# Kernel optimization log

Measured on AMD Instinct MI355X. Metric: run time of the kernel, lower is better.

## Reference

```python
import jax, jax.numpy as jnp
import numpy as np
import math

EMBED_DIM = 512
D_K = 64
D_V = 64
B, S = 4, 4096


def setup_inputs() -> dict:
    key = jax.random.key(0)
    ks = jax.random.split(key, 9)
    s = 1.0 / math.sqrt(EMBED_DIM)
    return {
        "query_in": jax.random.normal(ks[0], (B, S, EMBED_DIM), jnp.float32),
        "key_in": jax.random.normal(ks[1], (B, S, EMBED_DIM), jnp.float32),
        "value_in": jax.random.normal(ks[2], (B, S, EMBED_DIM), jnp.float32),
        "Wq": jax.random.normal(ks[3], (EMBED_DIM, D_K), jnp.float32) * s,
        "bq": jnp.zeros((D_K,), jnp.float32),
        "Wk": jax.random.normal(ks[4], (EMBED_DIM, D_K), jnp.float32) * s,
        "bk": jnp.zeros((D_K,), jnp.float32),
        "Wv": jax.random.normal(ks[5], (EMBED_DIM, D_V), jnp.float32) * s,
        "bv": jnp.zeros((D_V,), jnp.float32),
    }


def reference(query_in, key_in, value_in, Wq, bq, Wk, bk, Wv, bv):
    # Linear projections (value computed for faithfulness; unused by the
    # truncated forward, which returns pre-softmax scaled scores)
    q = query_in @ Wq + bq            # [B,S,d_k]
    k = key_in @ Wk + bk              # [B,S,d_k]
    v = value_in @ Wv + bv            # [B,S,d_v] (unused downstream)
    # scaled dot-product scores: Q K^T / sqrt(d_k)  -> [B,S,S]
    scores = jnp.einsum("bqd,bkd->bqk", q, k) / math.sqrt(D_K)
    return scores
```

## Files before the change

### kernel.cpp

```cpp
#include <hip/hip_runtime.h>

constexpr int Bn = 4;
constexpr int S  = 4096;
constexpr int E  = 512;
constexpr int DK = 64;
constexpr int XS_STRIDE = DK + 8;

typedef __attribute__((ext_vector_type(8))) short   bf16x8;
typedef __attribute__((ext_vector_type(4))) float   f32x4;

__device__ __forceinline__ unsigned short f2bf(float f) {
    unsigned x = __builtin_bit_cast(unsigned, f);
    unsigned r = x + 0x7FFFu + ((x >> 16) & 1u);
    return (unsigned short)(r >> 16);
}

__device__ __forceinline__ bf16x8 load8_f2bf(const float* __restrict__ p) {
    f32x4 a = *(const f32x4*)p;
    f32x4 b = *(const f32x4*)(p + 4);
    bf16x8 o;
    o[0] = (short)f2bf(a[0]); o[1] = (short)f2bf(a[1]);
    o[2] = (short)f2bf(a[2]); o[3] = (short)f2bf(a[3]);
    o[4] = (short)f2bf(b[0]); o[5] = (short)f2bf(b[1]);
    o[6] = (short)f2bf(b[2]); o[7] = (short)f2bf(b[3]);
    return o;
}

__global__ __launch_bounds__(256) void wt_kernel(const float* __restrict__ Wq,
                                                 const float* __restrict__ Wk,
                                                 unsigned short* __restrict__ Wt) {
    int idx = blockIdx.x * 256 + threadIdx.x;
    const float* W = blockIdx.y ? Wk : Wq;
    int n = idx >> 9;
    int k = idx & 511;
    Wt[blockIdx.y * (DK * E) + idx] = f2bf(W[k * DK + n]);
}

__global__ __launch_bounds__(256) void proj_kernel(const float* __restrict__ Xq,
                                                   const float* __restrict__ Xk,
                                                   const unsigned short* __restrict__ Wt,
                                                   const float* __restrict__ bq,
                                                   const float* __restrict__ bk,
                                                   unsigned short* __restrict__ Qp,
                                                   unsigned short* __restrict__ Kp) {
    const float*          X    = blockIdx.y ? Xk : Xq;
    const unsigned short* Wtm  = Wt + (size_t)blockIdx.y * DK * E;
    const float*          bias = blockIdx.y ? bk : bq;
    unsigned short*       P    = blockIdx.y ? Kp : Qp;

    __shared__ unsigned short xs[32][XS_STRIDE];

    const int tid  = threadIdx.x;
    const int wave = tid >> 6;
    const int lane = tid & 63;
    const int quad = lane >> 4;
    const int l16  = lane & 15;
    const long row0 = (long)blockIdx.x * 32;

    const int wrt = (wave & 1) * 16;
    const int wct = (wave >> 1) * 32;

    const int sr = tid >> 3;
    const int sk = (tid & 7) * 8;
    const float* xsrc = &X[(row0 + sr) * E + sk];

    f32x4 acc[2];
    acc[0] = (f32x4){0.f, 0.f, 0.f, 0.f};
    acc[1] = (f32x4){0.f, 0.f, 0.f, 0.f};

    for (int k0 = 0; k0 < E; k0 += 64) {
        __syncthreads();
        *(bf16x8*)&xs[sr][sk] = load8_f2bf(xsrc + k0);
        __syncthreads();

        bf16x8 bfrag[2][2];
#pragma unroll
        for (int kc = 0; kc < 2; ++kc)
#pragma unroll
            for (int ct = 0; ct < 2; ++ct)
                bfrag[kc][ct] = *(const bf16x8*)&Wtm[(size_t)(wct + ct * 16 + l16) * E + k0 + kc * 32 + quad * 8];

#pragma unroll
        for (int kc = 0; kc < 2; ++kc) {
            bf16x8 af = *(const bf16x8*)&xs[wrt + l16][kc * 32 + quad * 8];
            acc[0] = __builtin_amdgcn_mfma_f32_16x16x32_bf16(af, bfrag[kc][0], acc[0], 0, 0, 0);
            acc[1] = __builtin_amdgcn_mfma_f32_16x16x32_bf16(af, bfrag[kc][1], acc[1], 0, 0, 0);
        }
    }

#pragma unroll
    for (int ct = 0; ct < 2; ++ct) {
        float bv = bias[wct + ct * 16 + l16];
#pragma unroll
        for (int r = 0; r < 4; ++r) {
            long row = row0 + wrt + quad * 4 + r;
            P[row * DK + wct + ct * 16 + l16] = f2bf(acc[ct][r] + bv);
        }
    }
}

__global__ __launch_bounds__(256) void score_kernel(const unsigned short* __restrict__ Q,
                                                    const unsigned short* __restrict__ K,
                                                    float* __restrict__ out) {
    __shared__ __align__(16) char smraw[2 * 128 * XS_STRIDE * 2];
    unsigned short (*qs)[XS_STRIDE] = (unsigned short(*)[XS_STRIDE])smraw;
    unsigned short (*ks)[XS_STRIDE] = (unsigned short(*)[XS_STRIDE])(smraw + 128 * XS_STRIDE * 2);

    const int tid  = threadIdx.x;
    const int wave = tid >> 6;
    const int lane = tid & 63;
    const int quad = lane >> 4;
    const int l16  = lane & 15;

    const int  b     = blockIdx.z;
    const long qrow0 = (long)blockIdx.y * 128;
    const long krow0 = (long)blockIdx.x * 128;
    const unsigned short* Qb = Q + (size_t)b * S * DK;
    const unsigned short* Kb = K + (size_t)b * S * DK;

#pragma unroll
    for (int c = tid; c < 1024; c += 256) {
        int r  = c >> 3;
        int kc = (c & 7) * 8;
        *(bf16x8*)&qs[r][kc] = *(const bf16x8*)&Qb[(qrow0 + r) * DK + kc];
        *(bf16x8*)&ks[r][kc] = *(const bf16x8*)&Kb[(krow0 + r) * DK + kc];
    }
    __syncthreads();

    const int wr = wave * 32;

    bf16x8 afrag[2][2];
#pragma unroll
    for (int rt = 0; rt < 2; ++rt)
#pragma unroll
        for (int kc = 0; kc < 2; ++kc)
            afrag[rt][kc] = *(const bf16x8*)&qs[wr + rt * 16 + l16][kc * 32 + quad * 8];

    f32x4 acc[2][8];
#pragma unroll
    for (int rt = 0; rt < 2; ++rt)
#pragma unroll
        for (int ct = 0; ct < 8; ++ct) acc[rt][ct] = (f32x4){0.f, 0.f, 0.f, 0.f};

#pragma unroll
    for (int ct = 0; ct < 8; ++ct) {
        bf16x8 b0 = *(const bf16x8*)&ks[ct * 16 + l16][quad * 8];
        bf16x8 b1 = *(const bf16x8*)&ks[ct * 16 + l16][32 + quad * 8];
#pragma unroll
        for (int rt = 0; rt < 2; ++rt) {
            acc[rt][ct] = __builtin_amdgcn_mfma_f32_16x16x32_bf16(afrag[rt][0], b0, acc[rt][ct], 0, 0, 0);
            acc[rt][ct] = __builtin_amdgcn_mfma_f32_16x16x32_bf16(afrag[rt][1], b1, acc[rt][ct], 0, 0, 0);
        }
    }

    __syncthreads();

    float (*wbuf)[132] = (float(*)[132])(smraw + (size_t)wave * (16 * 132 * 4));

    float* ob = out + (size_t)b * S * S;
    const int rrow = lane >> 3;
    const int rcol = (lane & 7) * 4;

#pragma unroll
    for (int rt = 0; rt < 2; ++rt) {
#pragma unroll
        for (int ct = 0; ct < 8; ++ct)
#pragma unroll
            for (int r = 0; r < 4; ++r)
                wbuf[quad * 4 + r][ct * 16 + l16] = acc[rt][ct][r] * 0.125f;

#pragma unroll
        for (int jr = 0; jr < 2; ++jr)
#pragma unroll
            for (int jc = 0; jc < 4; ++jc) {
                int rr = jr * 8 + rrow;
                int cc = jc * 32 + rcol;
                f32x4 v = *(const f32x4*)&wbuf[rr][cc];
                *(f32x4*)&ob[(qrow0 + wr + rt * 16 + rr) * S + krow0 + cc] = v;
            }
    }
}

extern "C" void kernel_launch(void* const* d_in, const int* in_sizes, int n_in,
                              void* d_out, int out_size, void* d_ws, size_t ws_size,
                              hipStream_t stream) {
    (void)in_sizes; (void)n_in; (void)out_size; (void)ws_size;

    const float* query = (const float*)d_in[0];
    const float* key   = (const float*)d_in[1];
    const float* Wq    = (const float*)d_in[3];
    const float* bq    = (const float*)d_in[4];
    const float* Wk    = (const float*)d_in[5];
    const float* bk    = (const float*)d_in[6];

    unsigned short* ws = (unsigned short*)d_ws;
    unsigned short* Wt = ws;
    unsigned short* Qp = ws + 2 * DK * E;
    unsigned short* Kp = Qp + (size_t)Bn * S * DK;

    float* scores = (float*)d_out;

    wt_kernel<<<dim3(128, 2), 256, 0, stream>>>(Wq, Wk, Wt);
    proj_kernel<<<dim3(Bn * S / 32, 2), 256, 0, stream>>>(query, key, Wt, bq, bk, Qp, Kp);
    score_kernel<<<dim3(S / 128, S / 128, Bn), 256, 0, stream>>>(Qp, Kp, scores);
}
```

Before: 352.2 us.

## Load score operands straight from global, stage full X rows, use nontemporal stores

The score kernel no longer stages the Q and K tiles through LDS. It reads MFMA fragments directly from global memory, which removes the tile load and the barrier, and it uses a per-wave staging buffer only for the output transpose. Output stores become nontemporal so the large fp32 score matrix does not pollute the cache. The projection kernel now loads the whole 32x512 X block into LDS once instead of looping with paired barriers, which enlarges shared memory use and may lower occupancy.

```diff
diff --git a/kernel.cpp b/kernel.cpp
--- a/kernel.cpp
+++ b/kernel.cpp
@@ -4,7 +4,7 @@
 constexpr int S  = 4096;
 constexpr int E  = 512;
 constexpr int DK = 64;
-constexpr int XS_STRIDE = DK + 8;
+constexpr int XS_STRIDE = E + 8;
 
 typedef __attribute__((ext_vector_type(8))) short   bf16x8;
 typedef __attribute__((ext_vector_type(4))) float   f32x4;
@@ -60,19 +60,21 @@
     const int wrt = (wave & 1) * 16;
     const int wct = (wave >> 1) * 32;
 
-    const int sr = tid >> 3;
-    const int sk = (tid & 7) * 8;
-    const float* xsrc = &X[(row0 + sr) * E + sk];
+#pragma unroll
+    for (int i = 0; i < 8; ++i) {
+        int c = tid + 256 * i;
+        int r  = c >> 6;
+        int kc = (c & 63) * 8;
+        *(bf16x8*)&xs[r][kc] = load8_f2bf(&X[(row0 + r) * E + kc]);
+    }
+    __syncthreads();
 
     f32x4 acc[2];
     acc[0] = (f32x4){0.f, 0.f, 0.f, 0.f};
     acc[1] = (f32x4){0.f, 0.f, 0.f, 0.f};
 
+#pragma unroll
     for (int k0 = 0; k0 < E; k0 += 64) {
-        __syncthreads();
-        *(bf16x8*)&xs[sr][sk] = load8_f2bf(xsrc + k0);
-        __syncthreads();
-
         bf16x8 bfrag[2][2];
 #pragma unroll
         for (int kc = 0; kc < 2; ++kc)
@@ -82,7 +84,7 @@
 
 #pragma unroll
         for (int kc = 0; kc < 2; ++kc) {
-            bf16x8 af = *(const bf16x8*)&xs[wrt + l16][kc * 32 + quad * 8];
+            bf16x8 af = *(const bf16x8*)&xs[wrt + l16][k0 + kc * 32 + quad * 8];
             acc[0] = __builtin_amdgcn_mfma_f32_16x16x32_bf16(af, bfrag[kc][0], acc[0], 0, 0, 0);
             acc[1] = __builtin_amdgcn_mfma_f32_16x16x32_bf16(af, bfrag[kc][1], acc[1], 0, 0, 0);
         }
@@ -102,9 +104,7 @@
 __global__ __launch_bounds__(256) void score_kernel(const unsigned short* __restrict__ Q,
                                                     const unsigned short* __restrict__ K,
                                                     float* __restrict__ out) {
-    __shared__ __align__(16) char smraw[2 * 128 * XS_STRIDE * 2];
-    unsigned short (*qs)[XS_STRIDE] = (unsigned short(*)[XS_STRIDE])smraw;
-    unsigned short (*ks)[XS_STRIDE] = (unsigned short(*)[XS_STRIDE])(smraw + 128 * XS_STRIDE * 2);
+    __shared__ float wbuf4[4][16][132];
 
     const int tid  = threadIdx.x;
     const int wave = tid >> 6;
@@ -118,15 +118,6 @@
     const unsigned short* Qb = Q + (size_t)b * S * DK;
     const unsigned short* Kb = K + (size_t)b * S * DK;
 
-#pragma unroll
-    for (int c = tid; c < 1024; c += 256) {
-        int r  = c >> 3;
-        int kc = (c & 7) * 8;
-        *(bf16x8*)&qs[r][kc] = *(const bf16x8*)&Qb[(qrow0 + r) * DK + kc];
-        *(bf16x8*)&ks[r][kc] = *(const bf16x8*)&Kb[(krow0 + r) * DK + kc];
-    }
-    __syncthreads();
-
     const int wr = wave * 32;
 
     bf16x8 afrag[2][2];
@@ -134,7 +125,7 @@
     for (int rt = 0; rt < 2; ++rt)
 #pragma unroll
         for (int kc = 0; kc < 2; ++kc)
-            afrag[rt][kc] = *(const bf16x8*)&qs[wr + rt * 16 + l16][kc * 32 + quad * 8];
+            afrag[rt][kc] = *(const bf16x8*)&Qb[(qrow0 + wr + rt * 16 + l16) * DK + kc * 32 + quad * 8];
 
     f32x4 acc[2][8];
 #pragma unroll
@@ -144,8 +135,8 @@
 
 #pragma unroll
     for (int ct = 0; ct < 8; ++ct) {
-        bf16x8 b0 = *(const bf16x8*)&ks[ct * 16 + l16][quad * 8];
-        bf16x8 b1 = *(const bf16x8*)&ks[ct * 16 + l16][32 + quad * 8];
+        bf16x8 b0 = *(const bf16x8*)&Kb[(krow0 + ct * 16 + l16) * DK + quad * 8];
+        bf16x8 b1 = *(const bf16x8*)&Kb[(krow0 + ct * 16 + l16) * DK + 32 + quad * 8];
 #pragma unroll
         for (int rt = 0; rt < 2; ++rt) {
             acc[rt][ct] = __builtin_amdgcn_mfma_f32_16x16x32_bf16(afrag[rt][0], b0, acc[rt][ct], 0, 0, 0);
@@ -153,9 +144,7 @@
         }
     }
 
-    __syncthreads();
-
-    float (*wbuf)[132] = (float(*)[132])(smraw + (size_t)wave * (16 * 132 * 4));
+    float (*wbuf)[132] = wbuf4[wave];
 
     float* ob = out + (size_t)b * S * S;
     const int rrow = lane >> 3;
@@ -176,7 +165,7 @@
                 int rr = jr * 8 + rrow;
                 int cc = jc * 32 + rcol;
                 f32x4 v = *(const f32x4*)&wbuf[rr][cc];
-                *(f32x4*)&ob[(qrow0 + wr + rt * 16 + rr) * S + krow0 + cc] = v;
+                __builtin_nontemporal_store(v, (f32x4*)&ob[(qrow0 + wr + rt * 16 + rr) * S + krow0 + cc]);
             }
     }
 }
```

New measurement: 358.6 us. About the same (+1.8%).
